# Kernel tuning notes

Measured on AMD Instinct MI355X. Metric: run time of the kernel, lower is better.

Reference implementation:

```python
import jax, jax.numpy as jnp
import numpy as np

N_HEADS = 16


def _rope(x, sin, cos):
    # x: [B, H, T, D]; sin/cos: [1, 1, T, D]
    x1 = x[..., ::2]
    x2 = x[..., 1::2]
    xr = jnp.stack((-x2, x1), axis=-1).reshape(x.shape)
    return x * cos + xr * sin


def setup_inputs() -> dict:
    key = jax.random.key(0)
    k_x, k_s, k_c, k_w1, k_w2 = jax.random.split(key, 5)
    B, T, C = 4, 2048, 2048
    hd = C // N_HEADS
    x = jax.random.normal(k_x, (B, T, C), dtype=jnp.float32)
    sin = jax.random.uniform(k_s, (1, 1, T, hd), dtype=jnp.float32)
    cos = jax.random.uniform(k_c, (1, 1, T, hd), dtype=jnp.float32)
    W_qkv = jax.random.normal(k_w1, (C, 3 * C), dtype=jnp.float32) * 0.02
    W_proj = jax.random.normal(k_w2, (C, C), dtype=jnp.float32) * 0.02
    return {"x": x, "sin": sin, "cos": cos, "W_qkv": W_qkv, "W_proj": W_proj}


def reference(x, sin, cos, W_qkv, W_proj):
    B, T, C = x.shape
    hd = C // N_HEADS
    qkv = x @ W_qkv  # [B, T, 3C]
    q, k, v = jnp.split(qkv, 3, axis=-1)
    # [B, T, C] -> [B, H, T, D]
    q = q.reshape(B, T, N_HEADS, hd).transpose(0, 2, 1, 3)
    k = k.reshape(B, T, N_HEADS, hd).transpose(0, 2, 1, 3)
    v = v.reshape(B, T, N_HEADS, hd).transpose(0, 2, 1, 3)
    q = _rope(q, sin[:, :, :T, :], cos[:, :, :T, :])
    k = _rope(k, sin[:, :, :T, :], cos[:, :, :T, :])
    scale = 1.0 / jnp.sqrt(jnp.asarray(hd, dtype=x.dtype))
    scores = jnp.einsum("bhqd,bhkd->bhqk", q, k) * scale
    causal = jnp.tril(jnp.ones((T, T), dtype=bool))
    scores = jnp.where(causal, scores, jnp.asarray(-jnp.inf, dtype=scores.dtype))
    attn = jax.nn.softmax(scores, axis=-1)
    y = jnp.einsum("bhqk,bhkd->bhqd", attn, v)  # [B, H, T, D]
    y = y.transpose(0, 2, 1, 3).reshape(B, T, C)
    return y @ W_proj
```

## Files before the change

kernel.cpp:

```cpp
#include <hip/hip_runtime.h>
#include <hip/hip_bf16.h>
#include <stdint.h>

typedef uint32_t u32;
typedef uint16_t u16;
typedef __attribute__((ext_vector_type(8))) short short8;
typedef __attribute__((ext_vector_type(4))) float floatx4;

#define NH 16
#define HD 128
#define TSEQ 2048
#define NB 4
#define CM 2048
#define MROWS (NB*TSEQ)
#define NQKV (3*CM)

__device__ __forceinline__ u16 f2bf(float f) {
    union { float f; u32 u; } v; v.f = f;
    return (u16)((v.u + 0x7fffu + ((v.u >> 16) & 1u)) >> 16);
}

__device__ __forceinline__ void gload16(const u16* g, u16* l) {
    __builtin_amdgcn_global_load_lds(
        (const __attribute__((address_space(1))) void*)g,
        (__attribute__((address_space(3))) void*)l, 16, 0, 0);
}

__global__ __launch_bounds__(256) void convert_x_kernel(const float* __restrict__ in,
                                                        u16* __restrict__ out) {
    int idx = (blockIdx.x * 256 + threadIdx.x) * 8;
    float4 a = *(const float4*)(in + idx);
    float4 b = *(const float4*)(in + idx + 4);
    union { u16 s[8]; uint4 v; } o;
    o.s[0] = f2bf(a.x); o.s[1] = f2bf(a.y); o.s[2] = f2bf(a.z); o.s[3] = f2bf(a.w);
    o.s[4] = f2bf(b.x); o.s[5] = f2bf(b.y); o.s[6] = f2bf(b.z); o.s[7] = f2bf(b.w);
    *(uint4*)(out + idx) = o.v;
}

__global__ __launch_bounds__(256) void transpose_bf_kernel(const float* __restrict__ in,
                                                           u16* __restrict__ out,
                                                           int R, int Cn) {
    __shared__ float tile[32][33];
    int tx = threadIdx.x, ty = threadIdx.y;
    int c0 = blockIdx.x * 32, r0 = blockIdx.y * 32;
#pragma unroll
    for (int i = 0; i < 4; i++)
        tile[ty + i * 8][tx] = in[(size_t)(r0 + ty + i * 8) * Cn + c0 + tx];
    __syncthreads();
#pragma unroll
    for (int i = 0; i < 4; i++)
        out[(size_t)(c0 + ty + i * 8) * R + r0 + tx] = f2bf(tile[tx][ty + i * 8]);
}

__global__ __launch_bounds__(256, 2) void gemm_qkv_rope(const u16* __restrict__ A,
                                                        const u16* __restrict__ BT,
                                                        const float* __restrict__ sinp,
                                                        const float* __restrict__ cosp,
                                                        u16* __restrict__ q_ws,
                                                        u16* __restrict__ k_ws,
                                                        u16* __restrict__ v_ws) {
    __shared__ u16 As[128 * 32];
    __shared__ u16 Bs[128 * 32];
    int tid = threadIdx.x;
    int w = tid >> 6, lane = tid & 63, quad = lane >> 4, l15 = lane & 15;
    int mw = (w >> 1) * 64, nw = (w & 1) * 64;
    int blk = blockIdx.x;
    int xcd = blk & 7, idx8 = blk >> 3;
    int rowBase = (xcd * 8 + (idx8 & 7)) * 128;
    int colBase = (idx8 >> 3) * 128;

    floatx4 acc[4][4];
#pragma unroll
    for (int mi = 0; mi < 4; mi++)
#pragma unroll
        for (int ni = 0; ni < 4; ni++) acc[mi][ni] = (floatx4){0.f, 0.f, 0.f, 0.f};

    const u16* Asrc[2]; const u16* Bsrc[2];
#pragma unroll
    for (int i = 0; i < 2; i++) {
        int row = (w * 2 + i) * 16 + (lane >> 2);
        int cb  = (lane & 3) ^ ((row >> 1) & 3);
        Asrc[i] = A + (size_t)(rowBase + row) * CM + cb * 8;
        Bsrc[i] = BT + (size_t)(colBase + row) * CM + cb * 8;
    }

    for (int k0 = 0; k0 < CM; k0 += 32) {
#pragma unroll
        for (int i = 0; i < 2; i++) {
            gload16(Asrc[i] + k0, &As[(w * 2 + i) * 512]);
            gload16(Bsrc[i] + k0, &Bs[(w * 2 + i) * 512]);
        }
        __syncthreads();
        short8 af[4], bf[4];
#pragma unroll
        for (int mi = 0; mi < 4; mi++) {
            int row = mw + mi * 16 + l15;
            int pb = quad ^ ((row >> 1) & 3);
            af[mi] = *(const short8*)(&As[row * 32 + pb * 8]);
        }
#pragma unroll
        for (int ni = 0; ni < 4; ni++) {
            int row = nw + ni * 16 + l15;
            int pb = quad ^ ((row >> 1) & 3);
            bf[ni] = *(const short8*)(&Bs[row * 32 + pb * 8]);
        }
#pragma unroll
        for (int mi = 0; mi < 4; mi++)
#pragma unroll
            for (int ni = 0; ni < 4; ni++)
                acc[mi][ni] = __builtin_amdgcn_mfma_f32_16x16x32_bf16(af[mi], bf[ni],
                                                                      acc[mi][ni], 0, 0, 0);
        __syncthreads();
    }

    const float inv_sqrt_hd = 0.08838834764831845f;
#pragma unroll
    for (int mi = 0; mi < 4; mi++) {
#pragma unroll
        for (int ni = 0; ni < 4; ni++) {
            int j = colBase + nw + ni * 16 + l15;
            int sec = j >> 11;
            int jj = j & 2047;
            int h = jj >> 7, d = jj & 127;
            if (sec == 2) {
                int r0 = rowBase + mw + mi * 16 + quad * 4;
                int b = r0 >> 11, t0 = r0 & 2047;
                union { u16 s[4]; uint2 v; } pk;
#pragma unroll
                for (int reg = 0; reg < 4; reg++) pk.s[reg] = f2bf(acc[mi][ni][reg]);
                *(uint2*)(&v_ws[((size_t)(b * NH + h) * HD + d) * TSEQ + t0]) = pk.v;
            } else {
#pragma unroll
                for (int reg = 0; reg < 4; reg++) {
                    int r = rowBase + mw + mi * 16 + quad * 4 + reg;
                    int b = r >> 11, t = r & 2047;
                    float v = acc[mi][ni][reg];
                    float partner = __shfl_xor(v, 1, 64);
                    size_t dsti = (size_t)((b * NH + h) * TSEQ + t) * HD + d;
                    float s = sinp[t * HD + d], c = cosp[t * HD + d];
                    float o = v * c + ((d & 1) ? partner * s : -partner * s);
                    if (sec == 0) o *= inv_sqrt_hd;
                    ((sec == 0) ? q_ws : k_ws)[dsti] = f2bf(o);
                }
            }
        }
    }
}

__global__ __launch_bounds__(512, 1) void attn_kernel(const u16* __restrict__ q_ws,
                                                      const u16* __restrict__ k_ws,
                                                      const u16* __restrict__ vt_ws,
                                                      u16* __restrict__ y_bf) {
    __shared__ u16 smem[16 * 1024];
    __shared__ u16 Ps[128 * 72];
    u16* Ks = smem;
    u16* Vt = smem + 8192;
    int tid = threadIdx.x;
    int w = tid >> 6, lane = tid & 63, quad = lane >> 4, l15 = lane & 15;
    int qt = 15 - (blockIdx.x >> 6);
    int bh = blockIdx.x & 63;
    int b = bh >> 4, h = bh & 15;
    const u16* Qg = q_ws + (size_t)bh * TSEQ * HD;
    const u16* Kg = k_ws + (size_t)bh * TSEQ * HD;
    const u16* Vg = vt_ws + (size_t)bh * HD * TSEQ;

    uint4 kreg[2], vreg[2];
#pragma unroll
    for (int j = 0; j < 2; j++) {
        int idx = j * 512 + tid;
        int key = idx >> 4, s = idx & 15;
        kreg[j] = *(const uint4*)(Kg + (size_t)key * HD + s * 8);
    }
#pragma unroll
    for (int j = 0; j < 2; j++) {
        int idx = j * 512 + tid;
        int d = idx >> 3, s = idx & 7;
        vreg[j] = *(const uint4*)(Vg + (size_t)d * TSEQ + s * 8);
    }

#pragma unroll
    for (int j = 0; j < 4; j++) {
        int idx = j * 512 + tid;
        int row = idx >> 4, s = idx & 15;
        uint4 qv = *(const uint4*)(Qg + (size_t)(qt * 128 + row) * HD + s * 8);
        *(uint4*)(&smem[s * 1024 + ((row ^ (s & 7)) * 8)]) = qv;
    }
    __syncthreads();
    short8 qf[4];
#pragma unroll
    for (int kk = 0; kk < 4; kk++) {
        int row = w * 16 + l15;
        int s = kk * 4 + quad;
        qf[kk] = *(const short8*)(&smem[s * 1024 + ((row ^ (s & 7)) * 8)]);
    }

    floatx4 O[8];
#pragma unroll
    for (int f = 0; f < 8; f++) O[f] = (floatx4){0.f, 0.f, 0.f, 0.f};
    float l_i[4];
#pragma unroll
    for (int g = 0; g < 4; g++) l_i[g] = 0.f;

    int ktmax = 2 * qt + 1;
    for (int kt = 0; kt <= ktmax; kt++) {
        __syncthreads();
#pragma unroll
        for (int j = 0; j < 2; j++) {
            int idx = j * 512 + tid;
            int key = idx >> 4, s = idx & 15;
            *(uint4*)(&Ks[s * 512 + ((key ^ (s & 7)) * 8)]) = kreg[j];
        }
#pragma unroll
        for (int j = 0; j < 2; j++) {
            int idx = j * 512 + tid;
            int d = idx >> 3, s = idx & 7;
            *(uint4*)(&Vt[s * 1024 + ((d ^ s) * 8)]) = vreg[j];
        }
        __syncthreads();
        if (kt < ktmax) {
            const u16* Ktg = Kg + (size_t)((kt + 1) * 64) * HD;
            const u16* Vtg = Vg + (kt + 1) * 64;
#pragma unroll
            for (int j = 0; j < 2; j++) {
                int idx = j * 512 + tid;
                int key = idx >> 4, s = idx & 15;
                kreg[j] = *(const uint4*)(Ktg + (size_t)key * HD + s * 8);
            }
#pragma unroll
            for (int j = 0; j < 2; j++) {
                int idx = j * 512 + tid;
                int d = idx >> 3, s = idx & 7;
                vreg[j] = *(const uint4*)(Vtg + (size_t)d * TSEQ + s * 8);
            }
        }

        floatx4 S[4];
#pragma unroll
        for (int nf = 0; nf < 4; nf++) {
            short8 bb[4];
#pragma unroll
            for (int kk = 0; kk < 4; kk++) {
                int s = kk * 4 + quad;
                int key = nf * 16 + l15;
                bb[kk] = *(const short8*)(&Ks[s * 512 + ((key ^ (s & 7)) * 8)]);
            }
            floatx4 a4 = (floatx4){0.f, 0.f, 0.f, 0.f};
#pragma unroll
            for (int kk = 0; kk < 4; kk++)
                a4 = __builtin_amdgcn_mfma_f32_16x16x32_bf16(qf[kk], bb[kk], a4, 0, 0, 0);
            S[nf] = a4;
        }
        if (kt >= 2 * qt) {
#pragma unroll
            for (int nf = 0; nf < 4; nf++) {
                int key = kt * 64 + nf * 16 + l15;
#pragma unroll
                for (int reg = 0; reg < 4; reg++) {
                    int query = qt * 128 + w * 16 + quad * 4 + reg;
                    if (key > query) S[nf][reg] = -1e4f;
                }
            }
        }
#pragma unroll
        for (int nf = 0; nf < 4; nf++)
#pragma unroll
            for (int reg = 0; reg < 4; reg++) {
                float p = __expf(S[nf][reg]);
                l_i[reg] += p;
                Ps[(w * 16 + quad * 4 + reg) * 72 + nf * 16 + l15] = f2bf(p);
            }
        short8 pa[2];
#pragma unroll
        for (int kk = 0; kk < 2; kk++)
            pa[kk] = *(const short8*)(&Ps[(w * 16 + l15) * 72 + kk * 32 + quad * 8]);
#pragma unroll
        for (int f = 0; f < 8; f++) {
            short8 vb[2];
#pragma unroll
            for (int kk = 0; kk < 2; kk++) {
                int s = kk * 4 + quad;
                int d = f * 16 + l15;
                vb[kk] = *(const short8*)(&Vt[s * 1024 + ((d ^ s) * 8)]);
            }
#pragma unroll
            for (int kk = 0; kk < 2; kk++)
                O[f] = __builtin_amdgcn_mfma_f32_16x16x32_bf16(pa[kk], vb[kk], O[f], 0, 0, 0);
        }
    }

    float inv[4];
#pragma unroll
    for (int reg = 0; reg < 4; reg++) {
        float l = l_i[reg];
#pragma unroll
        for (int off = 1; off < 16; off <<= 1) l += __shfl_xor(l, off, 64);
        inv[reg] = 1.0f / l;
    }
#pragma unroll
    for (int f = 0; f < 8; f++)
#pragma unroll
        for (int reg = 0; reg < 4; reg++) {
            int t = qt * 128 + w * 16 + quad * 4 + reg;
            int col = h * HD + f * 16 + l15;
            y_bf[(size_t)(b * TSEQ + t) * CM + col] = f2bf(O[f][reg] * inv[reg]);
        }
}

__global__ __launch_bounds__(256, 2) void gemm_proj(const u16* __restrict__ A,
                                                    const u16* __restrict__ BT,
                                                    float* __restrict__ out) {
    __shared__ u16 As[128 * 32];
    __shared__ u16 Bs[128 * 32];
    int tid = threadIdx.x;
    int w = tid >> 6, lane = tid & 63, quad = lane >> 4, l15 = lane & 15;
    int mw = (w >> 1) * 64, nw = (w & 1) * 64;
    int blk = blockIdx.x;
    int xcd = blk & 7, idx8 = blk >> 3;
    int rowBase = (xcd * 8 + (idx8 & 7)) * 128;
    int colBase = (idx8 >> 3) * 128;

    floatx4 acc[4][4];
#pragma unroll
    for (int mi = 0; mi < 4; mi++)
#pragma unroll
        for (int ni = 0; ni < 4; ni++) acc[mi][ni] = (floatx4){0.f, 0.f, 0.f, 0.f};

    const u16* Asrc[2]; const u16* Bsrc[2];
#pragma unroll
    for (int i = 0; i < 2; i++) {
        int row = (w * 2 + i) * 16 + (lane >> 2);
        int cb  = (lane & 3) ^ ((row >> 1) & 3);
        Asrc[i] = A + (size_t)(rowBase + row) * CM + cb * 8;
        Bsrc[i] = BT + (size_t)(colBase + row) * CM + cb * 8;
    }

    for (int k0 = 0; k0 < CM; k0 += 32) {
#pragma unroll
        for (int i = 0; i < 2; i++) {
            gload16(Asrc[i] + k0, &As[(w * 2 + i) * 512]);
            gload16(Bsrc[i] + k0, &Bs[(w * 2 + i) * 512]);
        }
        __syncthreads();
        short8 af[4], bf[4];
#pragma unroll
        for (int mi = 0; mi < 4; mi++) {
            int row = mw + mi * 16 + l15;
            int pb = quad ^ ((row >> 1) & 3);
            af[mi] = *(const short8*)(&As[row * 32 + pb * 8]);
        }
#pragma unroll
        for (int ni = 0; ni < 4; ni++) {
            int row = nw + ni * 16 + l15;
            int pb = quad ^ ((row >> 1) & 3);
            bf[ni] = *(const short8*)(&Bs[row * 32 + pb * 8]);
        }
#pragma unroll
        for (int mi = 0; mi < 4; mi++)
#pragma unroll
            for (int ni = 0; ni < 4; ni++)
                acc[mi][ni] = __builtin_amdgcn_mfma_f32_16x16x32_bf16(af[mi], bf[ni],
                                                                      acc[mi][ni], 0, 0, 0);
        __syncthreads();
    }

#pragma unroll
    for (int mi = 0; mi < 4; mi++) {
#pragma unroll
        for (int ni = 0; ni < 4; ni++) {
            int j = colBase + nw + ni * 16 + l15;
#pragma unroll
            for (int reg = 0; reg < 4; reg++) {
                int r = rowBase + mw + mi * 16 + quad * 4 + reg;
                out[(size_t)r * CM + j] = acc[mi][ni][reg];
            }
        }
    }
}

extern "C" void kernel_launch(void* const* d_in, const int* in_sizes, int n_in,
                              void* d_out, int out_size, void* d_ws, size_t ws_size,
                              hipStream_t stream) {
    const float* x      = (const float*)d_in[0];
    const float* sinp   = (const float*)d_in[1];
    const float* cosp   = (const float*)d_in[2];
    const float* W_qkv  = (const float*)d_in[3];
    const float* W_proj = (const float*)d_in[4];
    float* out = (float*)d_out;

    char* ws = (char*)d_ws;
    size_t off = 0;
    u16* x_bf   = (u16*)(ws + off); off += (size_t)MROWS * CM * 2;
    u16* wqkvT  = (u16*)(ws + off); off += (size_t)NQKV * CM * 2;
    u16* wprojT = (u16*)(ws + off); off += (size_t)CM * CM * 2;
    u16* q_ws   = (u16*)(ws + off); off += (size_t)MROWS * CM * 2;
    u16* k_ws   = (u16*)(ws + off); off += (size_t)MROWS * CM * 2;
    u16* v_ws   = (u16*)(ws + off); off += (size_t)MROWS * CM * 2;
    u16* y_bf   = x_bf;

    convert_x_kernel<<<(MROWS * CM) / (256 * 8), 256, 0, stream>>>(x, x_bf);
    transpose_bf_kernel<<<dim3(NQKV / 32, CM / 32), dim3(32, 8), 0, stream>>>(W_qkv, wqkvT, CM, NQKV);
    transpose_bf_kernel<<<dim3(CM / 32, CM / 32), dim3(32, 8), 0, stream>>>(W_proj, wprojT, CM, CM);
    gemm_qkv_rope<<<(NQKV / 128) * (MROWS / 128), 256, 0, stream>>>(x_bf, wqkvT, sinp, cosp,
                                                                    q_ws, k_ws, v_ws);
    attn_kernel<<<(TSEQ / 128) * 64, 512, 0, stream>>>(q_ws, k_ws, v_ws, y_bf);
    gemm_proj<<<(CM / 128) * (MROWS / 128), 256, 0, stream>>>(y_bf, wprojT, out);
}
```

Baseline: 718.4 us.

## Use 256x256 double-buffered GEMM core with 512 threads for QKV and projection

Replaces the 128x128, 32-deep-K GEMM loops with a shared 256x256 tile core using 64-deep K steps, LDS double buffering, and interleaved async global-to-LDS loads between MFMA phases with raw barriers and wave priority hints. The aim is more data reuse per byte loaded and load latency hidden behind matrix math in both the QKV+RoPE and output projection kernels. In exchange it uses 128 KB of LDS and many accumulator registers per block, which limits occupancy to one block per CU, and relies on hand-placed barriers and waitcnts whose correctness is subtle.

```diff
diff --git a/kernel.cpp b/kernel.cpp
--- a/kernel.cpp
+++ b/kernel.cpp
@@ -52,78 +52,151 @@
         out[(size_t)(c0 + ty + i * 8) * R + r0 + tx] = f2bf(tile[tx][ty + i * 8]);
 }
 
-__global__ __launch_bounds__(256, 2) void gemm_qkv_rope(const u16* __restrict__ A,
+__device__ __forceinline__ void gemm256_core(const u16* __restrict__ A,
+                                             const u16* __restrict__ BT,
+                                             int rowBase, int colBase,
+                                             int tid, u16* lds,
+                                             floatx4 acc[8][4]) {
+    const int w = tid >> 6, lane = tid & 63, quad = lane >> 4, l15 = lane & 15;
+    const int wr = w >> 2, wc = w & 3;
+
+    const int srow = tid >> 3;
+    const int sl = (tid & 7) ^ (srow & 7);
+    const u16* aSrc[2][2]; const u16* bSrc[2][2];
+#pragma unroll
+    for (int h = 0; h < 2; h++)
+#pragma unroll
+        for (int j = 0; j < 2; j++) {
+            int r = h * 128 + j * 64 + srow;
+            aSrc[h][j] = A  + (size_t)(rowBase + r) * CM + sl * 8;
+            bSrc[h][j] = BT + (size_t)(colBase + r) * CM + sl * 8;
+        }
+    const int wofs = w * 512;
+
+    const int sA0 = (quad ^ (l15 & 7)) * 8;
+    const int sA1 = ((4 + quad) ^ (l15 & 7)) * 8;
+    u16* aBase = lds + wr * 8192;
+    u16* bBase = lds + 16384 + (wc >> 1) * 8192;
+    const int rB0 = (wc & 1) * 64;
+
+#define STAGE_A(q, kt) do { \
+    gload16(aSrc[0][0] + (kt) * 64, lds + (q) * 32768 + 0    + 0 * 4096 + wofs); \
+    gload16(aSrc[0][1] + (kt) * 64, lds + (q) * 32768 + 0    + 1 * 4096 + wofs); \
+    gload16(aSrc[1][0] + (kt) * 64, lds + (q) * 32768 + 8192 + 0 * 4096 + wofs); \
+    gload16(aSrc[1][1] + (kt) * 64, lds + (q) * 32768 + 8192 + 1 * 4096 + wofs); \
+} while (0)
+#define STAGE_B(q, kt) do { \
+    gload16(bSrc[0][0] + (kt) * 64, lds + (q) * 32768 + 16384 + 0 * 4096 + wofs); \
+    gload16(bSrc[0][1] + (kt) * 64, lds + (q) * 32768 + 16384 + 1 * 4096 + wofs); \
+    gload16(bSrc[1][0] + (kt) * 64, lds + (q) * 32768 + 24576 + 0 * 4096 + wofs); \
+    gload16(bSrc[1][1] + (kt) * 64, lds + (q) * 32768 + 24576 + 1 * 4096 + wofs); \
+} while (0)
+#define RAW_BARRIER() asm volatile("s_barrier" ::: "memory")
+
+    STAGE_A(0, 0); STAGE_B(0, 0);
+    asm volatile("s_waitcnt vmcnt(0)" ::: "memory");
+    RAW_BARRIER();
+
+    const int T = CM / 64;
+    for (int kt = 0; kt < T; kt++) {
+        const int p = kt & 1, q = p ^ 1;
+        const int pofs = p * 32768;
+        const bool pre = (kt + 1 < T);
+        short8 af[8], b0, b1;
+
+        if (pre) STAGE_A(q, kt + 1);
+#pragma unroll
+        for (int mi = 0; mi < 8; mi++)
+            af[mi] = *(const short8*)(aBase + pofs + (mi * 16 + l15) * 64 + sA0);
+        b0 = *(const short8*)(bBase + pofs + (rB0 + l15) * 64 + sA0);
+        b1 = *(const short8*)(bBase + pofs + (rB0 + 16 + l15) * 64 + sA0);
+        RAW_BARRIER();
+        __builtin_amdgcn_s_setprio(1);
+#pragma unroll
+        for (int mi = 0; mi < 8; mi++) {
+            acc[mi][0] = __builtin_amdgcn_mfma_f32_16x16x32_bf16(af[mi], b0, acc[mi][0], 0, 0, 0);
+            acc[mi][1] = __builtin_amdgcn_mfma_f32_16x16x32_bf16(af[mi], b1, acc[mi][1], 0, 0, 0);
+        }
+        __builtin_amdgcn_s_setprio(0);
+
+        if (pre) STAGE_B(q, kt + 1);
+        b0 = *(const short8*)(bBase + pofs + (rB0 + 32 + l15) * 64 + sA0);
+        b1 = *(const short8*)(bBase + pofs + (rB0 + 48 + l15) * 64 + sA0);
+        RAW_BARRIER();
+        __builtin_amdgcn_s_setprio(1);
+#pragma unroll
+        for (int mi = 0; mi < 8; mi++) {
+            acc[mi][2] = __builtin_amdgcn_mfma_f32_16x16x32_bf16(af[mi], b0, acc[mi][2], 0, 0, 0);
+            acc[mi][3] = __builtin_amdgcn_mfma_f32_16x16x32_bf16(af[mi], b1, acc[mi][3], 0, 0, 0);
+        }
+        __builtin_amdgcn_s_setprio(0);
+
+#pragma unroll
+        for (int mi = 0; mi < 8; mi++)
+            af[mi] = *(const short8*)(aBase + pofs + (mi * 16 + l15) * 64 + sA1);
+        b0 = *(const short8*)(bBase + pofs + (rB0 + l15) * 64 + sA1);
+        b1 = *(const short8*)(bBase + pofs + (rB0 + 16 + l15) * 64 + sA1);
+        RAW_BARRIER();
+        __builtin_amdgcn_s_setprio(1);
+#pragma unroll
+        for (int mi = 0; mi < 8; mi++) {
+            acc[mi][0] = __builtin_amdgcn_mfma_f32_16x16x32_bf16(af[mi], b0, acc[mi][0], 0, 0, 0);
+            acc[mi][1] = __builtin_amdgcn_mfma_f32_16x16x32_bf16(af[mi], b1, acc[mi][1], 0, 0, 0);
+        }
+        __builtin_amdgcn_s_setprio(0);
+
+        b0 = *(const short8*)(bBase + pofs + (rB0 + 32 + l15) * 64 + sA1);
+        b1 = *(const short8*)(bBase + pofs + (rB0 + 48 + l15) * 64 + sA1);
+        if (pre) asm volatile("s_waitcnt vmcnt(0)" ::: "memory");
+        RAW_BARRIER();
+        __builtin_amdgcn_s_setprio(1);
+#pragma unroll
+        for (int mi = 0; mi < 8; mi++) {
+            acc[mi][2] = __builtin_amdgcn_mfma_f32_16x16x32_bf16(af[mi], b0, acc[mi][2], 0, 0, 0);
+            acc[mi][3] = __builtin_amdgcn_mfma_f32_16x16x32_bf16(af[mi], b1, acc[mi][3], 0, 0, 0);
+        }
+        __builtin_amdgcn_s_setprio(0);
+    }
+#undef STAGE_A
+#undef STAGE_B
+#undef RAW_BARRIER
+}
+
+__global__ __launch_bounds__(512, 2) void gemm_qkv_rope(const u16* __restrict__ A,
                                                         const u16* __restrict__ BT,
                                                         const float* __restrict__ sinp,
                                                         const float* __restrict__ cosp,
                                                         u16* __restrict__ q_ws,
                                                         u16* __restrict__ k_ws,
                                                         u16* __restrict__ v_ws) {
-    __shared__ u16 As[128 * 32];
-    __shared__ u16 Bs[128 * 32];
+    __shared__ u16 lds[65536];
     int tid = threadIdx.x;
+    int blk = blockIdx.x;
+    int xcd = blk & 7, idx = blk >> 3;
+    int rowBase = (xcd * 4 + (idx & 3)) * 256;
+    int colBase = (idx >> 2) * 256;
+
+    floatx4 acc[8][4];
+#pragma unroll
+    for (int mi = 0; mi < 8; mi++)
+#pragma unroll
+        for (int ni = 0; ni < 4; ni++) acc[mi][ni] = (floatx4){0.f, 0.f, 0.f, 0.f};
+
+    gemm256_core(A, BT, rowBase, colBase, tid, lds, acc);
+
     int w = tid >> 6, lane = tid & 63, quad = lane >> 4, l15 = lane & 15;
-    int mw = (w >> 1) * 64, nw = (w & 1) * 64;
-    int blk = blockIdx.x;
-    int xcd = blk & 7, idx8 = blk >> 3;
-    int rowBase = (xcd * 8 + (idx8 & 7)) * 128;
-    int colBase = (idx8 >> 3) * 128;
-
-    floatx4 acc[4][4];
-#pragma unroll
-    for (int mi = 0; mi < 4; mi++)
-#pragma unroll
-        for (int ni = 0; ni < 4; ni++) acc[mi][ni] = (floatx4){0.f, 0.f, 0.f, 0.f};
-
-    const u16* Asrc[2]; const u16* Bsrc[2];
-#pragma unroll
-    for (int i = 0; i < 2; i++) {
-        int row = (w * 2 + i) * 16 + (lane >> 2);
-        int cb  = (lane & 3) ^ ((row >> 1) & 3);
-        Asrc[i] = A + (size_t)(rowBase + row) * CM + cb * 8;
-        Bsrc[i] = BT + (size_t)(colBase + row) * CM + cb * 8;
-    }
-
-    for (int k0 = 0; k0 < CM; k0 += 32) {
-#pragma unroll
-        for (int i = 0; i < 2; i++) {
-            gload16(Asrc[i] + k0, &As[(w * 2 + i) * 512]);
-            gload16(Bsrc[i] + k0, &Bs[(w * 2 + i) * 512]);
-        }
-        __syncthreads();
-        short8 af[4], bf[4];
-#pragma unroll
-        for (int mi = 0; mi < 4; mi++) {
-            int row = mw + mi * 16 + l15;
-            int pb = quad ^ ((row >> 1) & 3);
-            af[mi] = *(const short8*)(&As[row * 32 + pb * 8]);
-        }
+    int wr = w >> 2, wc = w & 3;
+    const float inv_sqrt_hd = 0.08838834764831845f;
+#pragma unroll
+    for (int mi = 0; mi < 8; mi++) {
 #pragma unroll
         for (int ni = 0; ni < 4; ni++) {
-            int row = nw + ni * 16 + l15;
-            int pb = quad ^ ((row >> 1) & 3);
-            bf[ni] = *(const short8*)(&Bs[row * 32 + pb * 8]);
-        }
-#pragma unroll
-        for (int mi = 0; mi < 4; mi++)
-#pragma unroll
-            for (int ni = 0; ni < 4; ni++)
-                acc[mi][ni] = __builtin_amdgcn_mfma_f32_16x16x32_bf16(af[mi], bf[ni],
-                                                                      acc[mi][ni], 0, 0, 0);
-        __syncthreads();
-    }
-
-    const float inv_sqrt_hd = 0.08838834764831845f;
-#pragma unroll
-    for (int mi = 0; mi < 4; mi++) {
-#pragma unroll
-        for (int ni = 0; ni < 4; ni++) {
-            int j = colBase + nw + ni * 16 + l15;
+            int j = colBase + wc * 64 + ni * 16 + l15;
             int sec = j >> 11;
             int jj = j & 2047;
             int h = jj >> 7, d = jj & 127;
             if (sec == 2) {
-                int r0 = rowBase + mw + mi * 16 + quad * 4;
+                int r0 = rowBase + wr * 128 + mi * 16 + quad * 4;
                 int b = r0 >> 11, t0 = r0 & 2047;
                 union { u16 s[4]; uint2 v; } pk;
 #pragma unroll
@@ -132,7 +205,7 @@
             } else {
 #pragma unroll
                 for (int reg = 0; reg < 4; reg++) {
-                    int r = rowBase + mw + mi * 16 + quad * 4 + reg;
+                    int r = rowBase + wr * 128 + mi * 16 + quad * 4 + reg;
                     int b = r >> 11, t = r & 2047;
                     float v = acc[mi][ni][reg];
                     float partner = __shfl_xor(v, 1, 64);
@@ -142,6 +215,40 @@
                     if (sec == 0) o *= inv_sqrt_hd;
                     ((sec == 0) ? q_ws : k_ws)[dsti] = f2bf(o);
                 }
+            }
+        }
+    }
+}
+
+__global__ __launch_bounds__(512, 2) void gemm_proj(const u16* __restrict__ A,
+                                                    const u16* __restrict__ BT,
+                                                    float* __restrict__ out) {
+    __shared__ u16 lds[65536];
+    int tid = threadIdx.x;
+    int blk = blockIdx.x;
+    int xcd = blk & 7, idx = blk >> 3;
+    int rowBase = (xcd * 4 + (idx & 3)) * 256;
+    int colBase = (idx >> 2) * 256;
+
+    floatx4 acc[8][4];
+#pragma unroll
+    for (int mi = 0; mi < 8; mi++)
+#pragma unroll
+        for (int ni = 0; ni < 4; ni++) acc[mi][ni] = (floatx4){0.f, 0.f, 0.f, 0.f};
+
+    gemm256_core(A, BT, rowBase, colBase, tid, lds, acc);
+
+    int w = tid >> 6, lane = tid & 63, quad = lane >> 4, l15 = lane & 15;
+    int wr = w >> 2, wc = w & 3;
+#pragma unroll
+    for (int mi = 0; mi < 8; mi++) {
+#pragma unroll
+        for (int ni = 0; ni < 4; ni++) {
+            int j = colBase + wc * 64 + ni * 16 + l15;
+#pragma unroll
+            for (int reg = 0; reg < 4; reg++) {
+                int r = rowBase + wr * 128 + mi * 16 + quad * 4 + reg;
+                out[(size_t)r * CM + j] = acc[mi][ni][reg];
             }
         }
     }
@@ -230,7 +337,7 @@
             for (int j = 0; j < 2; j++) {
                 int idx = j * 512 + tid;
                 int d = idx >> 3, s = idx & 7;
-                vreg[j] = *(const uint4*)(Vtg + (size_t)d * TSEQ + s * 8);
+                vreg[j] = *(const uint4*)(Vtg + (size_t)(d) * TSEQ + s * 8);
             }
         }
 
@@ -304,77 +411,6 @@
             int col = h * HD + f * 16 + l15;
             y_bf[(size_t)(b * TSEQ + t) * CM + col] = f2bf(O[f][reg] * inv[reg]);
         }
-}
-
-__global__ __launch_bounds__(256, 2) void gemm_proj(const u16* __restrict__ A,
-                                                    const u16* __restrict__ BT,
-                                                    float* __restrict__ out) {
-    __shared__ u16 As[128 * 32];
-    __shared__ u16 Bs[128 * 32];
-    int tid = threadIdx.x;
-    int w = tid >> 6, lane = tid & 63, quad = lane >> 4, l15 = lane & 15;
-    int mw = (w >> 1) * 64, nw = (w & 1) * 64;
-    int blk = blockIdx.x;
-    int xcd = blk & 7, idx8 = blk >> 3;
-    int rowBase = (xcd * 8 + (idx8 & 7)) * 128;
-    int colBase = (idx8 >> 3) * 128;
-
-    floatx4 acc[4][4];
-#pragma unroll
-    for (int mi = 0; mi < 4; mi++)
-#pragma unroll
-        for (int ni = 0; ni < 4; ni++) acc[mi][ni] = (floatx4){0.f, 0.f, 0.f, 0.f};
-
-    const u16* Asrc[2]; const u16* Bsrc[2];
-#pragma unroll
-    for (int i = 0; i < 2; i++) {
-        int row = (w * 2 + i) * 16 + (lane >> 2);
-        int cb  = (lane & 3) ^ ((row >> 1) & 3);
-        Asrc[i] = A + (size_t)(rowBase + row) * CM + cb * 8;
-        Bsrc[i] = BT + (size_t)(colBase + row) * CM + cb * 8;
-    }
-
-    for (int k0 = 0; k0 < CM; k0 += 32) {
-#pragma unroll
-        for (int i = 0; i < 2; i++) {
-            gload16(Asrc[i] + k0, &As[(w * 2 + i) * 512]);
-            gload16(Bsrc[i] + k0, &Bs[(w * 2 + i) * 512]);
-        }
-        __syncthreads();
-        short8 af[4], bf[4];
-#pragma unroll
-        for (int mi = 0; mi < 4; mi++) {
-            int row = mw + mi * 16 + l15;
-            int pb = quad ^ ((row >> 1) & 3);
-            af[mi] = *(const short8*)(&As[row * 32 + pb * 8]);
-        }
-#pragma unroll
-        for (int ni = 0; ni < 4; ni++) {
-            int row = nw + ni * 16 + l15;
-            int pb = quad ^ ((row >> 1) & 3);
-            bf[ni] = *(const short8*)(&Bs[row * 32 + pb * 8]);
-        }
-#pragma unroll
-        for (int mi = 0; mi < 4; mi++)
-#pragma unroll
-            for (int ni = 0; ni < 4; ni++)
-                acc[mi][ni] = __builtin_amdgcn_mfma_f32_16x16x32_bf16(af[mi], bf[ni],
-                                                                      acc[mi][ni], 0, 0, 0);
-        __syncthreads();
-    }
-
-#pragma unroll
-    for (int mi = 0; mi < 4; mi++) {
-#pragma unroll
-        for (int ni = 0; ni < 4; ni++) {
-            int j = colBase + nw + ni * 16 + l15;
-#pragma unroll
-            for (int reg = 0; reg < 4; reg++) {
-                int r = rowBase + mw + mi * 16 + quad * 4 + reg;
-                out[(size_t)r * CM + j] = acc[mi][ni][reg];
-            }
-        }
-    }
 }
 
 extern "C" void kernel_launch(void* const* d_in, const int* in_sizes, int n_in,
@@ -400,8 +436,8 @@
     convert_x_kernel<<<(MROWS * CM) / (256 * 8), 256, 0, stream>>>(x, x_bf);
     transpose_bf_kernel<<<dim3(NQKV / 32, CM / 32), dim3(32, 8), 0, stream>>>(W_qkv, wqkvT, CM, NQKV);
     transpose_bf_kernel<<<dim3(CM / 32, CM / 32), dim3(32, 8), 0, stream>>>(W_proj, wprojT, CM, CM);
-    gemm_qkv_rope<<<(NQKV / 128) * (MROWS / 128), 256, 0, stream>>>(x_bf, wqkvT, sinp, cosp,
+    gemm_qkv_rope<<<(MROWS / 256) * (NQKV / 256), 512, 0, stream>>>(x_bf, wqkvT, sinp, cosp,
                                                                     q_ws, k_ws, v_ws);
     attn_kernel<<<(TSEQ / 128) * 64, 512, 0, stream>>>(q_ws, k_ws, v_ws, y_bf);
-    gemm_proj<<<(CM / 128) * (MROWS / 128), 256, 0, stream>>>(y_bf, wprojT, out);
-}
+    gemm_proj<<<(MROWS / 256) * (CM / 256), 512, 0, stream>>>(y_bf, wprojT, out);
+}
```

Result: faster. 656.4 us (-8.6%).
